# Kernel optimization log

Hardware: AMD Instinct MI355X
Metric: run time of the kernel (lower is better)

## Reference

```python
import jax, jax.numpy as jnp
import numpy as np

N, D, L, E = 50000, 128, 4, 300000  # nodes, feat dim, layers, edges per hop


def setup_inputs() -> dict:
    key = jax.random.key(0)
    ks = jax.random.split(key, 8)
    scale = 1.0 / np.sqrt(D).astype(np.float32)
    x = jax.random.normal(ks[0], (N, D), jnp.float32)
    W1 = jax.random.normal(ks[1], (L, D, D), jnp.float32) * scale
    b1 = jnp.zeros((L, D), jnp.float32)
    W2 = jax.random.normal(ks[2], (L, D, D), jnp.float32) * scale
    b2 = jnp.zeros((L, D), jnp.float32)
    alpha = jax.random.normal(ks[3], (L, 2), jnp.float32)
    src1 = jax.random.randint(ks[4], (E,), 0, N, jnp.int32)
    dst1 = jax.random.randint(ks[5], (E,), 0, N, jnp.int32)
    src2 = jax.random.randint(ks[6], (E,), 0, N, jnp.int32)
    dst2 = jax.random.randint(ks[7], (E,), 0, N, jnp.int32)
    return dict(x=x, W1=W1, b1=b1, W2=W2, b2=b2, alpha=alpha,
                src1=src1, dst1=dst1, src2=src2, dst2=dst2)


def _edge_norm(src, dst, n):
    # symmetric GCN normalization per edge: deg_out(src)^-1/2 * deg_in(dst)^-1/2
    ones = jnp.ones(src.shape[0], jnp.float32)
    deg_out = jax.ops.segment_sum(ones, src, num_segments=n)
    deg_in = jax.ops.segment_sum(ones, dst, num_segments=n)
    inv_out = jnp.where(deg_out > 0, jax.lax.rsqrt(jnp.maximum(deg_out, 1.0)), 0.0)
    inv_in = jnp.where(deg_in > 0, jax.lax.rsqrt(jnp.maximum(deg_in, 1.0)), 0.0)
    return inv_out[src] * inv_in[dst]  # [E]


def _gcn(x, W, b, src, dst, norm):
    # GCNConv: scatter-add of normalized, linearly transformed source features
    h = x @ W                                   # [N, D]
    msg = h[src] * norm[:, None]                # [E, D] gather
    out = jax.ops.segment_sum(msg, dst, num_segments=x.shape[0])
    return out + b


def reference(x, W1, b1, W2, b2, alpha, src1, dst1, src2, dst2):
    n = x.shape[0]
    norm1 = _edge_norm(src1, dst1, n)
    norm2 = _edge_norm(src2, dst2, n)
    xs = []
    for t in range(L):
        xs.append(x)
        if t == 0:
            # only the 1-hop neighbourhood is active; softmax over 1 element = 1
            a = jax.nn.softmax(alpha[0, :1])
            agg = a[0] * _gcn(xs[t], W1[t], b1[t], src1, dst1, norm1)
        else:
            a = jax.nn.softmax(alpha[t])
            # k=1: no delay; k=2 with nu=1: delay = max(2-1, 0) = 1 -> x[t-1]
            agg = (a[0] * _gcn(xs[t], W1[t], b1[t], src1, dst1, norm1)
                   + a[1] * _gcn(xs[t - 1], W2[t], b2[t], src2, dst2, norm2))
        x = xs[t] + jax.nn.relu(agg)            # residual + ReLU
        # F.normalize(p=2, dim=-1), eps=1e-12
        x = x / jnp.maximum(jnp.linalg.norm(x, axis=-1, keepdims=True), 1e-12)
    return x
```

## Files before the change

kernel.cpp:

```cpp
#include <hip/hip_runtime.h>


typedef unsigned short u16;
typedef __attribute__((ext_vector_type(8))) short short8;
typedef __attribute__((ext_vector_type(8))) unsigned short ushort8;
typedef __attribute__((ext_vector_type(4))) float f32x4;

__device__ inline float bf2f(u16 u) {
  return __uint_as_float(((unsigned int)u) << 16);
}
__device__ inline u16 f2bf(float f) {
  unsigned int u = __float_as_uint(f);
  return (u16)((u + 0x7fff + ((u >> 16) & 1)) >> 16);
}

__global__ __launch_bounds__(256) void init_k(
    const float* __restrict__ x_in, const float* __restrict__ W1,
    const float* __restrict__ W2, const float* __restrict__ alpha,
    int* __restrict__ cnt, u16* __restrict__ xb0,
    u16* __restrict__ wt1, u16* __restrict__ wt2,
    float* __restrict__ a_soft, int N, int Lnum) {
  int gtid = blockIdx.x * 256 + threadIdx.x;
  int gsz = gridDim.x * 256;
  for (int i = gtid; i < 4 * N; i += gsz) cnt[i] = 0;
  int n8 = N * 16;
  for (int id = gtid; id < n8; id += gsz) {
    const float4* q = (const float4*)(x_in + (size_t)id * 8);
    float4 v0 = q[0], v1 = q[1];
    ushort8 o;
    o[0] = f2bf(v0.x); o[1] = f2bf(v0.y); o[2] = f2bf(v0.z); o[3] = f2bf(v0.w);
    o[4] = f2bf(v1.x); o[5] = f2bf(v1.y); o[6] = f2bf(v1.z); o[7] = f2bf(v1.w);
    *(ushort8*)(xb0 + (size_t)id * 8) = o;
  }
  for (int id = gtid; id < 2 * Lnum * 4096; id += gsz) {
    int mat = id >> 12, rem = id & 4095;
    int k = rem >> 5, n4 = (rem & 31) * 4;
    const float* W = (mat < Lnum) ? (W1 + (size_t)mat * 16384)
                                  : (W2 + (size_t)(mat - Lnum) * 16384);
    u16* Wt = (mat < Lnum) ? (wt1 + (size_t)mat * 16384)
                           : (wt2 + (size_t)(mat - Lnum) * 16384);
    float4 v = *(const float4*)&W[k * 128 + n4];
    Wt[(size_t)(n4 + 0) * 128 + k] = f2bf(v.x);
    Wt[(size_t)(n4 + 1) * 128 + k] = f2bf(v.y);
    Wt[(size_t)(n4 + 2) * 128 + k] = f2bf(v.z);
    Wt[(size_t)(n4 + 3) * 128 + k] = f2bf(v.w);
  }
  if (blockIdx.x == 0 && threadIdx.x < Lnum) {
    int t = threadIdx.x;
    if (t == 0) { a_soft[0] = 1.0f; a_soft[1] = 0.0f; }
    else {
      float x0 = alpha[2 * t], x1 = alpha[2 * t + 1];
      float m = fmaxf(x0, x1);
      float e0 = expf(x0 - m), e1 = expf(x1 - m);
      float inv = 1.0f / (e0 + e1);
      a_soft[2 * t] = e0 * inv;
      a_soft[2 * t + 1] = e1 * inv;
    }
  }
}

__global__ __launch_bounds__(256) void deg_k(const int* __restrict__ src1,
                                             const int* __restrict__ dst1,
                                             const int* __restrict__ src2,
                                             const int* __restrict__ dst2,
                                             int* __restrict__ cnt,
                                             int N, int E1, int E2) {
  int i = threadIdx.x + blockIdx.x * 256;
  if (i < E1) {
    atomicAdd(&cnt[src1[i]], 1);
    atomicAdd(&cnt[N + dst1[i]], 1);
  }
  int j = i - E1;
  if (j >= 0 && j < E2) {
    atomicAdd(&cnt[2 * N + src2[j]], 1);
    atomicAdd(&cnt[3 * N + dst2[j]], 1);
  }
}

__global__ __launch_bounds__(256) void psum_k(
    const int* __restrict__ cnt, float* __restrict__ degs,
    const float* __restrict__ b1, const float* __restrict__ b2,
    const float* __restrict__ a_soft, float* __restrict__ bb,
    int* __restrict__ bsums, int N, int Lnum) {
  int gtid = blockIdx.x * 256 + threadIdx.x;
  int gsz = gridDim.x * 256;
  for (int i = gtid; i < 4 * N; i += gsz) {
    int v = cnt[i];
    degs[i] = (v > 0) ? rsqrtf((float)v) : 0.0f;
  }
  for (int id = gtid; id < Lnum * 128; id += gsz) {
    int t = id >> 7;
    bb[id] = a_soft[2 * t] * b1[id] + a_soft[2 * t + 1] * b2[id];
  }
  const int* cnti1 = cnt + N;
  const int* cnti2 = cnt + 3 * N;
  int base = blockIdx.x * 1024 + threadIdx.x * 4;
  int s = 0;
#pragma unroll
  for (int j = 0; j < 4; ++j) {
    int i = base + j;
    if (i < N) s += cnti1[i] + cnti2[i];
  }
#pragma unroll
  for (int off = 1; off < 64; off <<= 1) s += __shfl_xor(s, off, 64);
  __shared__ int ws[4];
  int lane = threadIdx.x & 63, w = threadIdx.x >> 6;
  if (lane == 0) ws[w] = s;
  __syncthreads();
  if (threadIdx.x == 0 && blockIdx.x * 1024 < N)
    bsums[blockIdx.x] = ws[0] + ws[1] + ws[2] + ws[3];
}

__global__ __launch_bounds__(256) void bscan_k(const int* __restrict__ bsums,
                                               int* __restrict__ boffs,
                                               int* __restrict__ row_start,
                                               int nb, int n) {
  __shared__ int sm[256];
  int tid = threadIdx.x;
  int v = (tid < nb) ? bsums[tid] : 0;
  sm[tid] = v;
  __syncthreads();
  for (int off = 1; off < 256; off <<= 1) {
    int u = (tid >= off) ? sm[tid - off] : 0;
    __syncthreads();
    sm[tid] += u;
    __syncthreads();
  }
  if (tid < nb) boffs[tid] = sm[tid] - v;
  if (tid == 255) row_start[n] = sm[255];
}

__global__ __launch_bounds__(256) void sapply_k(const int* __restrict__ cnt,
                                                const int* __restrict__ boffs,
                                                int* __restrict__ row_start,
                                                int* __restrict__ cursor, int N) {
  const int* cnti1 = cnt + N;
  const int* cnti2 = cnt + 3 * N;
  int lane = threadIdx.x & 63, w = threadIdx.x >> 6;
  int base = blockIdx.x * 1024 + threadIdx.x * 4;
  int c[4], s = 0;
#pragma unroll
  for (int j = 0; j < 4; ++j) {
    int i = base + j;
    c[j] = (i < N) ? (cnti1[i] + cnti2[i]) : 0;
    s += c[j];
  }
  int incl = s;
#pragma unroll
  for (int off = 1; off < 64; off <<= 1) {
    int u = __shfl_up(incl, off, 64);
    if (lane >= off) incl += u;
  }
  int excl = incl - s;
  __shared__ int ws[4];
  if (lane == 63) ws[w] = incl;
  __syncthreads();
  int woff = 0;
  for (int i = 0; i < w; ++i) woff += ws[i];
  int off0 = boffs[blockIdx.x] + woff + excl;
#pragma unroll
  for (int j = 0; j < 4; ++j) {
    int i = base + j;
    if (i < N) { row_start[i] = off0; cursor[i] = off0; off0 += c[j]; }
  }
}

__global__ __launch_bounds__(256) void place_k(const int* __restrict__ src,
                                               const int* __restrict__ dst,
                                               int* __restrict__ cursor,
                                               int* __restrict__ esrc,
                                               int soff, int E) {
  int i = threadIdx.x + blockIdx.x * 256;
  if (i >= E) return;
  int slot = atomicAdd(&cursor[dst[i]], 1);
  esrc[slot] = src[i] + soff;
}

__global__ __launch_bounds__(256) void gemm_dual_k(
    const u16* __restrict__ Xc, const u16* __restrict__ Xp,
    const u16* __restrict__ wt1, const u16* __restrict__ wt2,
    u16* __restrict__ h1, u16* __restrict__ h2,
    const float* __restrict__ invo1, const float* __restrict__ invo2,
    const float* __restrict__ a_soft, int t, int n, int gemmG) {
  int hop = (blockIdx.x >= gemmG) ? 1 : 0;
  int bid = blockIdx.x - hop * gemmG;
  const u16* __restrict__ Xb = hop ? Xp : Xc;
  const u16* __restrict__ Wt = hop ? wt2 : wt1;
  u16* __restrict__ H = hop ? h2 : h1;
  const float* __restrict__ invo = hop ? invo2 : invo1;
  int aidx = 2 * t + hop;

  __shared__ __align__(16) u16 wl[128 * 128];
  __shared__ __align__(16) u16 xl[64 * 128];
  int tid = threadIdx.x;
  int row0 = bid * 64;
  bool tail = (row0 + 64 > n);
#pragma unroll
  for (int j = 0; j < 8; ++j) {
    int c = tid + 256 * j;
    int row = c >> 4, col8 = (c & 15) * 8;
    ushort8 v = *(const ushort8*)&Wt[(size_t)row * 128 + col8];
    *(ushort8*)&wl[row * 128 + (col8 ^ ((row & 15) * 8))] = v;
  }
#pragma unroll
  for (int j = 0; j < 4; ++j) {
    int c = tid + 256 * j;
    int r = c >> 4, col8 = (c & 15) * 8;
    int rr = row0 + r;
    ushort8 v = (ushort8){0, 0, 0, 0, 0, 0, 0, 0};
    if (!tail || rr < n) v = *(const ushort8*)&Xb[(size_t)rr * 128 + col8];
    *(ushort8*)&xl[r * 128 + (col8 ^ ((r & 15) * 8))] = v;
  }
  __syncthreads();

  int lane = tid & 63, w = tid >> 6;
  int m15 = lane & 15, kg = lane >> 4;
  int xr = w * 16 + m15;

  f32x4 acc[8];
#pragma unroll
  for (int i = 0; i < 8; ++i) acc[i] = (f32x4){0.f, 0.f, 0.f, 0.f};

#pragma unroll
  for (int ks = 0; ks < 4; ++ks) {
    int bcol = (kg * 8 + ks * 32) ^ ((xr & 15) * 8);
    short8 bx = *(const short8*)&xl[xr * 128 + bcol];
#pragma unroll
    for (int fn = 0; fn < 8; ++fn) {
      int wrow = fn * 16 + m15;
      int wcol = (kg * 8 + ks * 32) ^ ((wrow & 15) * 8);
      short8 aw = *(const short8*)&wl[wrow * 128 + wcol];
      acc[fn] = __builtin_amdgcn_mfma_f32_16x16x32_bf16(aw, bx, acc[fn], 0, 0, 0);
    }
  }

  int grow = row0 + xr;
  if (grow < n) {
    float sc = a_soft[aidx] * invo[grow];
    u16* hrow = &H[(size_t)grow * 128];
#pragma unroll
    for (int fn = 0; fn < 8; ++fn) {
      ushort4 o;
      o.x = f2bf(acc[fn][0] * sc); o.y = f2bf(acc[fn][1] * sc);
      o.z = f2bf(acc[fn][2] * sc); o.w = f2bf(acc[fn][3] * sc);
      *(ushort4*)&hrow[fn * 16 + kg * 4] = o;
    }
  }
}

__device__ inline void fma_acc(float2* a, uint4 h, float sc) {
  a[0].x += sc * __uint_as_float(h.x << 16);
  a[0].y += sc * __uint_as_float(h.x & 0xffff0000u);
  a[1].x += sc * __uint_as_float(h.y << 16);
  a[1].y += sc * __uint_as_float(h.y & 0xffff0000u);
  a[2].x += sc * __uint_as_float(h.z << 16);
  a[2].y += sc * __uint_as_float(h.z & 0xffff0000u);
  a[3].x += sc * __uint_as_float(h.w << 16);
  a[3].y += sc * __uint_as_float(h.w & 0xffff0000u);
}

__global__ __launch_bounds__(256) void aggfin_k(
    const u16* __restrict__ Xb, const u16* __restrict__ H,
    const int* __restrict__ rs, const int* __restrict__ es,
    const int* __restrict__ d1arr,
    const float* __restrict__ invi1, const float* __restrict__ invi2,
    const float* __restrict__ bb,
    u16* __restrict__ XnB, float* __restrict__ XnF,
    int n, int hop2, int final_f32) {
  int w = threadIdx.x >> 6, lane = threadIdx.x & 63;
  int row = blockIdx.x * 4 + w;
  if (row >= n) return;
  int grp = lane >> 4, l16 = lane & 15;
  int c8 = l16 * 8;

  int e0 = rs[row];
  int eend = hop2 ? rs[row + 1] : (e0 + d1arr[row]);
  float gi1 = invi1[row], gi2 = invi2[row];

  float2 a[4] = {{0.f, 0.f}, {0.f, 0.f}, {0.f, 0.f}, {0.f, 0.f}};
  int e = e0 + grp;
  while (e + 12 < eend) {
    int s0 = es[e], s1 = es[e + 4], s2 = es[e + 8], s3 = es[e + 12];
    uint4 h0 = *(const uint4*)&H[(size_t)s0 * 128 + c8];
    uint4 h1 = *(const uint4*)&H[(size_t)s1 * 128 + c8];
    uint4 h2 = *(const uint4*)&H[(size_t)s2 * 128 + c8];
    uint4 h3 = *(const uint4*)&H[(size_t)s3 * 128 + c8];
    fma_acc(a, h0, (s0 >= n) ? gi2 : gi1);
    fma_acc(a, h1, (s1 >= n) ? gi2 : gi1);
    fma_acc(a, h2, (s2 >= n) ? gi2 : gi1);
    fma_acc(a, h3, (s3 >= n) ? gi2 : gi1);
    e += 16;
  }
  while (e + 4 < eend) {
    int s0 = es[e], s1 = es[e + 4];
    uint4 h0 = *(const uint4*)&H[(size_t)s0 * 128 + c8];
    uint4 h1 = *(const uint4*)&H[(size_t)s1 * 128 + c8];
    fma_acc(a, h0, (s0 >= n) ? gi2 : gi1);
    fma_acc(a, h1, (s1 >= n) ? gi2 : gi1);
    e += 8;
  }
  if (e < eend) {
    int s = es[e];
    uint4 h = *(const uint4*)&H[(size_t)s * 128 + c8];
    fma_acc(a, h, (s >= n) ? gi2 : gi1);
  }

  float t8[8] = {a[0].x, a[0].y, a[1].x, a[1].y, a[2].x, a[2].y, a[3].x, a[3].y};
#pragma unroll
  for (int j = 0; j < 8; ++j) t8[j] += __shfl_xor(t8[j], 16, 64);
#pragma unroll
  for (int j = 0; j < 8; ++j) t8[j] += __shfl_xor(t8[j], 32, 64);

  float4 bv0 = *(const float4*)&bb[c8];
  float4 bv1 = *(const float4*)&bb[c8 + 4];
  float bbv[8] = {bv0.x, bv0.y, bv0.z, bv0.w, bv1.x, bv1.y, bv1.z, bv1.w};
  ushort8 xv = *(const ushort8*)&Xb[(size_t)row * 128 + c8];
  float v[8];
  float ss = 0.f;
#pragma unroll
  for (int j = 0; j < 8; ++j) {
    v[j] = bf2f(xv[j]) + fmaxf(t8[j] + bbv[j], 0.f);
    ss += v[j] * v[j];
  }
#pragma unroll
  for (int off = 1; off <= 8; off <<= 1) ss += __shfl_xor(ss, off, 64);
  float inv = 1.0f / fmaxf(sqrtf(ss), 1e-12f);

  if (final_f32) {
    if (grp == 0) {
      *(float4*)&XnF[(size_t)row * 128 + c8] =
          make_float4(v[0] * inv, v[1] * inv, v[2] * inv, v[3] * inv);
      *(float4*)&XnF[(size_t)row * 128 + c8 + 4] =
          make_float4(v[4] * inv, v[5] * inv, v[6] * inv, v[7] * inv);
    }
  } else {
    if (grp == 0) {
      ushort8 o;
#pragma unroll
      for (int j = 0; j < 8; ++j) o[j] = f2bf(v[j] * inv);
      *(ushort8*)&XnB[(size_t)row * 128 + c8] = o;
    }
  }
}

extern "C" void kernel_launch(void* const* d_in, const int* in_sizes, int n_in,
                              void* d_out, int out_size, void* d_ws, size_t ws_size,
                              hipStream_t stream) {
  const float* x_in  = (const float*)d_in[0];
  const float* W1    = (const float*)d_in[1];
  const float* b1    = (const float*)d_in[2];
  const float* W2    = (const float*)d_in[3];
  const float* b2    = (const float*)d_in[4];
  const float* alpha = (const float*)d_in[5];
  const int* src1 = (const int*)d_in[6];
  const int* dst1 = (const int*)d_in[7];
  const int* src2 = (const int*)d_in[8];
  const int* dst2 = (const int*)d_in[9];

  int N = in_sizes[0] / 128;
  int Lnum = in_sizes[5] / 2;
  int E1 = in_sizes[6], E2 = in_sizes[8];

  size_t ND = (size_t)N * 128;
  u16* xb0 = (u16*)d_ws;
  u16* xbA = xb0 + ND;
  u16* xbB = xbA + ND;
  u16* h1  = xbB + ND;
  u16* h2  = h1 + ND;
  float* degs = (float*)(h2 + ND);
  float* a_soft = degs + 4 * (size_t)N;
  float* bb = a_soft + 64;
  int* cnt  = (int*)(bb + 512);
  int* rsc  = cnt + 4 * (size_t)N;
  int* curc = rsc + N + 1;
  int* bsum = curc + N;
  int* boff = bsum + 512;
  int* esc  = boff + 512;
  u16* wt1 = (u16*)((((uintptr_t)(esc + E1 + E2)) + 15) & ~(uintptr_t)15);
  u16* wt2 = wt1 + (size_t)Lnum * 16384;

  float* invo1 = degs;
  float* invi1 = degs + N;
  float* invo2 = degs + 2 * (size_t)N;
  float* invi2 = degs + 3 * (size_t)N;
  int* cnti1 = cnt + N;

  int nb = (N + 1023) / 1024;

  init_k<<<1024, 256, 0, stream>>>(x_in, W1, W2, alpha, cnt, xb0, wt1, wt2,
                                   a_soft, N, Lnum);
  deg_k<<<(E1 + E2 + 255) / 256, 256, 0, stream>>>(src1, dst1, src2, dst2,
                                                   cnt, N, E1, E2);
  psum_k<<<nb, 256, 0, stream>>>(cnt, degs, b1, b2, a_soft, bb, bsum, N, Lnum);
  bscan_k<<<1, 256, 0, stream>>>(bsum, boff, rsc, nb, N);
  sapply_k<<<nb, 256, 0, stream>>>(cnt, boff, rsc, curc, N);
  place_k<<<(E1 + 255) / 256, 256, 0, stream>>>(src1, dst1, curc, esc, 0, E1);
  place_k<<<(E2 + 255) / 256, 256, 0, stream>>>(src2, dst2, curc, esc, N, E2);

  float* out = (float*)d_out;
  int gemmG = (N + 63) / 64;
  int fin_grid = (N + 3) / 4;

  u16* xbuf[8];
  xbuf[0] = xb0; xbuf[1] = xbA; xbuf[2] = xbB;
  for (int i = 3; i < 8; ++i) xbuf[i] = xbuf[i - 3];

  for (int t = 0; t < Lnum; ++t) {
    const u16* cur = xbuf[t];
    const u16* prev = (t > 0) ? xbuf[t - 1] : cur;
    int fin = (t == Lnum - 1);
    u16* nxt = fin ? nullptr : xbuf[t + 1];
    int grid = (t > 0) ? 2 * gemmG : gemmG;
    gemm_dual_k<<<grid, 256, 0, stream>>>(cur, prev,
                                          wt1 + (size_t)t * 16384,
                                          wt2 + (size_t)t * 16384,
                                          h1, h2, invo1, invo2,
                                          a_soft, t, N, gemmG);
    aggfin_k<<<fin_grid, 256, 0, stream>>>(cur, h1, rsc, esc, cnti1,
                                           invi1, invi2, bb + (size_t)t * 128,
                                           nxt, out, N, t > 0 ? 1 : 0, fin);
  }
}
```

Baseline: 292.2 us.

## Merge CSR preprocessing kernels and give each lane group a contiguous edge range

Degree counting moves into init_k behind a hipMemsetAsync. The block-offset scan is folded into sapply_k with a wave-level scan, and the two place_k launches become one, with separate per-hop cursors so hop-1 edges come before hop-2 edges in each row. The aggregation kernel now gives each of the four edge groups a contiguous quarter of the row instead of a stride-4 interleave, which should make index loads more sequential. This cuts several launches, at the cost of the wave-scan assuming no more than 64 blocks (nb).

```diff
diff --git a/kernel.cpp b/kernel.cpp
--- a/kernel.cpp
+++ b/kernel.cpp
@@ -17,12 +17,21 @@
 __global__ __launch_bounds__(256) void init_k(
     const float* __restrict__ x_in, const float* __restrict__ W1,
     const float* __restrict__ W2, const float* __restrict__ alpha,
+    const int* __restrict__ src1, const int* __restrict__ dst1,
+    const int* __restrict__ src2, const int* __restrict__ dst2,
     int* __restrict__ cnt, u16* __restrict__ xb0,
     u16* __restrict__ wt1, u16* __restrict__ wt2,
-    float* __restrict__ a_soft, int N, int Lnum) {
+    float* __restrict__ a_soft, int N, int Lnum, int E1, int E2) {
   int gtid = blockIdx.x * 256 + threadIdx.x;
   int gsz = gridDim.x * 256;
-  for (int i = gtid; i < 4 * N; i += gsz) cnt[i] = 0;
+  for (int i = gtid; i < E1; i += gsz) {
+    atomicAdd(&cnt[src1[i]], 1);
+    atomicAdd(&cnt[N + dst1[i]], 1);
+  }
+  for (int i = gtid; i < E2; i += gsz) {
+    atomicAdd(&cnt[2 * N + src2[i]], 1);
+    atomicAdd(&cnt[3 * N + dst2[i]], 1);
+  }
   int n8 = N * 16;
   for (int id = gtid; id < n8; id += gsz) {
     const float4* q = (const float4*)(x_in + (size_t)id * 8);
@@ -59,24 +68,6 @@
   }
 }
 
-__global__ __launch_bounds__(256) void deg_k(const int* __restrict__ src1,
-                                             const int* __restrict__ dst1,
-                                             const int* __restrict__ src2,
-                                             const int* __restrict__ dst2,
-                                             int* __restrict__ cnt,
-                                             int N, int E1, int E2) {
-  int i = threadIdx.x + blockIdx.x * 256;
-  if (i < E1) {
-    atomicAdd(&cnt[src1[i]], 1);
-    atomicAdd(&cnt[N + dst1[i]], 1);
-  }
-  int j = i - E1;
-  if (j >= 0 && j < E2) {
-    atomicAdd(&cnt[2 * N + src2[j]], 1);
-    atomicAdd(&cnt[3 * N + dst2[j]], 1);
-  }
-}
-
 __global__ __launch_bounds__(256) void psum_k(
     const int* __restrict__ cnt, float* __restrict__ degs,
     const float* __restrict__ b1, const float* __restrict__ b2,
@@ -107,42 +98,40 @@
   int lane = threadIdx.x & 63, w = threadIdx.x >> 6;
   if (lane == 0) ws[w] = s;
   __syncthreads();
-  if (threadIdx.x == 0 && blockIdx.x * 1024 < N)
-    bsums[blockIdx.x] = ws[0] + ws[1] + ws[2] + ws[3];
-}
-
-__global__ __launch_bounds__(256) void bscan_k(const int* __restrict__ bsums,
-                                               int* __restrict__ boffs,
-                                               int* __restrict__ row_start,
-                                               int nb, int n) {
-  __shared__ int sm[256];
-  int tid = threadIdx.x;
-  int v = (tid < nb) ? bsums[tid] : 0;
-  sm[tid] = v;
-  __syncthreads();
-  for (int off = 1; off < 256; off <<= 1) {
-    int u = (tid >= off) ? sm[tid - off] : 0;
-    __syncthreads();
-    sm[tid] += u;
-    __syncthreads();
-  }
-  if (tid < nb) boffs[tid] = sm[tid] - v;
-  if (tid == 255) row_start[n] = sm[255];
-}
-
-__global__ __launch_bounds__(256) void sapply_k(const int* __restrict__ cnt,
-                                                const int* __restrict__ boffs,
-                                                int* __restrict__ row_start,
-                                                int* __restrict__ cursor, int N) {
+  if (threadIdx.x == 0) bsums[blockIdx.x] = ws[0] + ws[1] + ws[2] + ws[3];
+}
+
+__global__ __launch_bounds__(256) void sapply_k(
+    const int* __restrict__ cnt, const int* __restrict__ bsums,
+    int* __restrict__ row_start, int* __restrict__ cur1,
+    int* __restrict__ cur2, int N, int nb) {
   const int* cnti1 = cnt + N;
   const int* cnti2 = cnt + 3 * N;
   int lane = threadIdx.x & 63, w = threadIdx.x >> 6;
+  __shared__ int boff_sm, total_sm;
+  __shared__ int ws[4];
+  if (threadIdx.x < 64) {
+    int v = (lane < nb) ? bsums[lane] : 0;
+    int incl = v;
+#pragma unroll
+    for (int off = 1; off < 64; off <<= 1) {
+      int u = __shfl_up(incl, off, 64);
+      if (lane >= off) incl += u;
+    }
+    int bid = blockIdx.x;
+    int bo = (bid == 0) ? 0 : __shfl(incl, bid - 1, 64);
+    int tot = __shfl(incl, nb - 1, 64);
+    if (lane == 0) { boff_sm = bo; total_sm = tot; }
+  }
+  __syncthreads();
+
   int base = blockIdx.x * 1024 + threadIdx.x * 4;
-  int c[4], s = 0;
+  int c[4], d1[4], s = 0;
 #pragma unroll
   for (int j = 0; j < 4; ++j) {
     int i = base + j;
-    c[j] = (i < N) ? (cnti1[i] + cnti2[i]) : 0;
+    d1[j] = (i < N) ? cnti1[i] : 0;
+    c[j] = (i < N) ? (d1[j] + cnti2[i]) : 0;
     s += c[j];
   }
   int incl = s;
@@ -152,28 +141,39 @@
     if (lane >= off) incl += u;
   }
   int excl = incl - s;
-  __shared__ int ws[4];
   if (lane == 63) ws[w] = incl;
   __syncthreads();
   int woff = 0;
   for (int i = 0; i < w; ++i) woff += ws[i];
-  int off0 = boffs[blockIdx.x] + woff + excl;
+  int off0 = boff_sm + woff + excl;
 #pragma unroll
   for (int j = 0; j < 4; ++j) {
     int i = base + j;
-    if (i < N) { row_start[i] = off0; cursor[i] = off0; off0 += c[j]; }
-  }
-}
-
-__global__ __launch_bounds__(256) void place_k(const int* __restrict__ src,
-                                               const int* __restrict__ dst,
-                                               int* __restrict__ cursor,
-                                               int* __restrict__ esrc,
-                                               int soff, int E) {
+    if (i < N) {
+      row_start[i] = off0;
+      cur1[i] = off0;
+      cur2[i] = off0 + d1[j];
+      off0 += c[j];
+    }
+  }
+  if (blockIdx.x == 0 && threadIdx.x == 0) row_start[N] = total_sm;
+}
+
+__global__ __launch_bounds__(256) void place_k(
+    const int* __restrict__ src1, const int* __restrict__ dst1,
+    const int* __restrict__ src2, const int* __restrict__ dst2,
+    int* __restrict__ cur1, int* __restrict__ cur2,
+    int* __restrict__ esrc, int N, int E1, int E2) {
   int i = threadIdx.x + blockIdx.x * 256;
-  if (i >= E) return;
-  int slot = atomicAdd(&cursor[dst[i]], 1);
-  esrc[slot] = src[i] + soff;
+  if (i < E1) {
+    int slot = atomicAdd(&cur1[dst1[i]], 1);
+    esrc[slot] = src1[i];
+  }
+  int j = i - E1;
+  if (j >= 0 && j < E2) {
+    int slot = atomicAdd(&cur2[dst2[j]], 1);
+    esrc[slot] = src2[j] + N;
+  }
 }
 
 __global__ __launch_bounds__(256) void gemm_dual_k(
@@ -274,13 +274,15 @@
   int c8 = l16 * 8;
 
   int e0 = rs[row];
-  int eend = hop2 ? rs[row + 1] : (e0 + d1arr[row]);
+  int len = hop2 ? (rs[row + 1] - e0) : d1arr[row];
   float gi1 = invi1[row], gi2 = invi2[row];
 
+  int gs = e0 + ((len * grp) >> 2);
+  int ge = e0 + ((len * (grp + 1)) >> 2);
+
   float2 a[4] = {{0.f, 0.f}, {0.f, 0.f}, {0.f, 0.f}, {0.f, 0.f}};
-  int e = e0 + grp;
-  while (e + 12 < eend) {
-    int s0 = es[e], s1 = es[e + 4], s2 = es[e + 8], s3 = es[e + 12];
+  while (gs + 3 < ge) {
+    int s0 = es[gs], s1 = es[gs + 1], s2 = es[gs + 2], s3 = es[gs + 3];
     uint4 h0 = *(const uint4*)&H[(size_t)s0 * 128 + c8];
     uint4 h1 = *(const uint4*)&H[(size_t)s1 * 128 + c8];
     uint4 h2 = *(const uint4*)&H[(size_t)s2 * 128 + c8];
@@ -289,18 +291,18 @@
     fma_acc(a, h1, (s1 >= n) ? gi2 : gi1);
     fma_acc(a, h2, (s2 >= n) ? gi2 : gi1);
     fma_acc(a, h3, (s3 >= n) ? gi2 : gi1);
-    e += 16;
-  }
-  while (e + 4 < eend) {
-    int s0 = es[e], s1 = es[e + 4];
+    gs += 4;
+  }
+  if (gs + 1 < ge) {
+    int s0 = es[gs], s1 = es[gs + 1];
     uint4 h0 = *(const uint4*)&H[(size_t)s0 * 128 + c8];
     uint4 h1 = *(const uint4*)&H[(size_t)s1 * 128 + c8];
     fma_acc(a, h0, (s0 >= n) ? gi2 : gi1);
     fma_acc(a, h1, (s1 >= n) ? gi2 : gi1);
-    e += 8;
-  }
-  if (e < eend) {
-    int s = es[e];
+    gs += 2;
+  }
+  if (gs < ge) {
+    int s = es[gs];
     uint4 h = *(const uint4*)&H[(size_t)s * 128 + c8];
     fma_acc(a, h, (s >= n) ? gi2 : gi1);
   }
@@ -372,10 +374,10 @@
   float* bb = a_soft + 64;
   int* cnt  = (int*)(bb + 512);
   int* rsc  = cnt + 4 * (size_t)N;
-  int* curc = rsc + N + 1;
-  int* bsum = curc + N;
-  int* boff = bsum + 512;
-  int* esc  = boff + 512;
+  int* cur1 = rsc + N + 1;
+  int* cur2 = cur1 + N;
+  int* bsum = cur2 + N;
+  int* esc  = bsum + 512;
   u16* wt1 = (u16*)((((uintptr_t)(esc + E1 + E2)) + 15) & ~(uintptr_t)15);
   u16* wt2 = wt1 + (size_t)Lnum * 16384;
 
@@ -387,15 +389,13 @@
 
   int nb = (N + 1023) / 1024;
 
-  init_k<<<1024, 256, 0, stream>>>(x_in, W1, W2, alpha, cnt, xb0, wt1, wt2,
-                                   a_soft, N, Lnum);
-  deg_k<<<(E1 + E2 + 255) / 256, 256, 0, stream>>>(src1, dst1, src2, dst2,
-                                                   cnt, N, E1, E2);
+  hipMemsetAsync(cnt, 0, 4 * (size_t)N * sizeof(int), stream);
+  init_k<<<1024, 256, 0, stream>>>(x_in, W1, W2, alpha, src1, dst1, src2, dst2,
+                                   cnt, xb0, wt1, wt2, a_soft, N, Lnum, E1, E2);
   psum_k<<<nb, 256, 0, stream>>>(cnt, degs, b1, b2, a_soft, bb, bsum, N, Lnum);
-  bscan_k<<<1, 256, 0, stream>>>(bsum, boff, rsc, nb, N);
-  sapply_k<<<nb, 256, 0, stream>>>(cnt, boff, rsc, curc, N);
-  place_k<<<(E1 + 255) / 256, 256, 0, stream>>>(src1, dst1, curc, esc, 0, E1);
-  place_k<<<(E2 + 255) / 256, 256, 0, stream>>>(src2, dst2, curc, esc, N, E2);
+  sapply_k<<<nb, 256, 0, stream>>>(cnt, bsum, rsc, cur1, cur2, N, nb);
+  place_k<<<(E1 + E2 + 255) / 256, 256, 0, stream>>>(src1, dst1, src2, dst2,
+                                                     cur1, cur2, esc, N, E1, E2);
 
   float* out = (float*)d_out;
   int gemmG = (N + 63) / 64;
```

Result: no change. 288.5 us (-1.3%).
